# Optimization experiments

Hardware: AMD Instinct MI355X
Metric: run time of the kernel (lower is better)

## Reference

```python
import jax, jax.numpy as jnp
import numpy as np

N, E, B = 50000, 800000, 64
D_IN, D_E = 192, 64
NUM_OUT = 256


def setup_inputs() -> dict:
    key = jax.random.key(0)
    ks = jax.random.split(key, 30)
    rn = lambda k, s: jax.random.normal(k, s, dtype=jnp.float32) * 0.05
    return {
        "x": jax.random.normal(ks[0], (N, D_IN), jnp.float32),
        "edge_index": jax.random.randint(ks[1], (2, E), 0, N, dtype=jnp.int32),
        "edge_attr": jax.random.normal(ks[2], (E, D_E), jnp.float32),
        "batch": jnp.sort(jax.random.randint(ks[3], (N,), 0, B, dtype=jnp.int32)),
        "W1": rn(ks[4], (D_IN, 256)), "as1": rn(ks[5], (4, 64)), "ad1": rn(ks[6], (4, 64)),
        "We1": rn(ks[7], (D_E, 256)), "ae1": rn(ks[8], (4, 64)), "b1": rn(ks[9], (256,)),
        "W2": rn(ks[10], (256, 256)), "as2": rn(ks[11], (4, 64)), "ad2": rn(ks[12], (4, 64)),
        "We2": rn(ks[13], (D_E, 256)), "ae2": rn(ks[14], (4, 64)), "b2": rn(ks[15], (256,)),
        "W3": rn(ks[16], (256, 512)), "as3": rn(ks[17], (4, 128)), "ad3": rn(ks[18], (4, 128)),
        "We3": rn(ks[19], (D_E, 512)), "ae3": rn(ks[20], (4, 128)), "b3": rn(ks[21], (128,)),
        "Wa": rn(ks[22], (128, NUM_OUT)), "ba": rn(ks[23], (NUM_OUT,)),
        "Wv": rn(ks[24], (128, 1)), "bv": rn(ks[25], (1,)),
    }


def reference(x, edge_index, edge_attr, batch,
              W1, as1, ad1, We1, ae1, b1,
              W2, as2, ad2, We2, ae2, b2,
              W3, as3, ad3, We3, ae3, b3,
              Wa, ba, Wv, bv):
    Nn = x.shape[0]
    src0, dst0 = edge_index[0], edge_index[1]
    # PyG add_self_loops(fill_value='mean'): self-loop edge_attr = mean of incoming edge_attr
    deg = jax.ops.segment_sum(jnp.ones_like(dst0, dtype=x.dtype), dst0, num_segments=Nn)
    loop_attr = jax.ops.segment_sum(edge_attr, dst0, num_segments=Nn) / jnp.maximum(deg, 1.0)[:, None]
    loop = jnp.arange(Nn, dtype=src0.dtype)
    src = jnp.concatenate([src0, loop])
    dst = jnp.concatenate([dst0, loop])
    ea = jnp.concatenate([edge_attr, loop_attr], axis=0)

    def gat(h, W, a_s, a_d, We, a_e, bias, concat):
        Hh, C = a_s.shape
        hs = (h @ W).reshape(Nn, Hh, C)                       # [N,H,C]
        al_s = (hs * a_s).sum(-1)                             # [N,H]
        al_d = (hs * a_d).sum(-1)                             # [N,H]
        al_e = ((ea @ We).reshape(-1, Hh, C) * a_e).sum(-1)   # [E+N,H]
        alpha = jax.nn.leaky_relu(al_s[src] + al_d[dst] + al_e, 0.2)
        amax = jax.ops.segment_max(alpha, dst, num_segments=Nn)
        w = jnp.exp(alpha - amax[dst])
        denom = jax.ops.segment_sum(w, dst, num_segments=Nn)
        w = w / (denom[dst] + 1e-16)                          # scatter-softmax over dst
        out = jax.ops.segment_sum(hs[src] * w[..., None], dst, num_segments=Nn)
        out = out.reshape(Nn, Hh * C) if concat else out.mean(axis=1)
        return out + bias

    h = jax.nn.relu(gat(x, W1, as1, ad1, We1, ae1, b1, True))
    h = jax.nn.relu(gat(h, W2, as2, ad2, We2, ae2, b2, True))
    h = gat(h, W3, as3, ad3, We3, ae3, b3, False)
    cnt = jax.ops.segment_sum(jnp.ones((Nn,), h.dtype), batch, num_segments=B)
    g = jax.ops.segment_sum(h, batch, num_segments=B) / jnp.maximum(cnt, 1.0)[:, None]
    logits = g @ Wa + ba
    value = g @ Wv + bv
    return jnp.concatenate([logits, value], axis=-1)  # [B, num_outputs+1]
```

## Files before the change

kernel.cpp:

```cpp
#include <hip/hip_runtime.h>
#include <hip/hip_bf16.h>


typedef __attribute__((ext_vector_type(8))) short short8;
typedef __attribute__((ext_vector_type(4))) float floatx4;

#define DEV __device__ __forceinline__

DEV unsigned short f2b(float f) {
  union { float f; unsigned u; } v; v.f = f;
  unsigned r = v.u + 0x7FFFu + ((v.u >> 16) & 1u);
  return (unsigned short)(r >> 16);
}
DEV float b2f(unsigned short u) {
  union { unsigned u; float f; } v; v.u = ((unsigned)u) << 16;
  return v.f;
}

__global__ void k_deg(const int* __restrict__ dst, int* __restrict__ deg, int E) {
  int e = blockIdx.x * 256 + threadIdx.x;
  if (e < E) atomicAdd(&deg[dst[e]], 1);
}

__global__ __launch_bounds__(256) void k_scan1(const int* __restrict__ deg,
    int* __restrict__ rowptr, int* __restrict__ bsum, int N) {
  __shared__ int sd[256];
  int b = blockIdx.x, tid = threadIdx.x;
  int i0 = b * 1024 + tid * 4;
  int v[4]; int s = 0;
#pragma unroll
  for (int j = 0; j < 4; j++) { int i = i0 + j; v[j] = (i < N) ? deg[i] : 0; s += v[j]; }
  sd[tid] = s;
  __syncthreads();
  for (int off = 1; off < 256; off <<= 1) {
    int t = (tid >= off) ? sd[tid - off] : 0;
    __syncthreads();
    sd[tid] += t;
    __syncthreads();
  }
  int run = sd[tid] - s;
#pragma unroll
  for (int j = 0; j < 4; j++) { int i = i0 + j; if (i < N) rowptr[i] = run; run += v[j]; }
  if (tid == 255) bsum[b] = sd[255];
}

__global__ __launch_bounds__(256) void k_scan2(int* __restrict__ bsum, int nb) {
  __shared__ int sd[256];
  int tid = threadIdx.x;
  int v = (tid < nb) ? bsum[tid] : 0;
  sd[tid] = v;
  __syncthreads();
  for (int off = 1; off < 256; off <<= 1) {
    int t = (tid >= off) ? sd[tid - off] : 0;
    __syncthreads();
    sd[tid] += t;
    __syncthreads();
  }
  if (tid < nb) bsum[tid] = sd[tid] - v;
}

__global__ __launch_bounds__(256) void k_scan3(int* __restrict__ rowptr,
    int* __restrict__ cursor, const int* __restrict__ bsum, int N, int E) {
  int b = blockIdx.x, tid = threadIdx.x;
  int add = bsum[b];
  int i0 = b * 1024 + tid * 4;
#pragma unroll
  for (int j = 0; j < 4; j++) {
    int i = i0 + j;
    if (i < N) { int r = rowptr[i] + add; rowptr[i] = r; cursor[i] = r; }
  }
  if (b == 0 && tid == 0) rowptr[N] = E;
}

__global__ void k_scatter(const int* __restrict__ src, const int* __restrict__ dst,
    int* __restrict__ cursor, int2* __restrict__ csr, int E) {
  int e = blockIdx.x * 256 + threadIdx.x;
  if (e < E) {
    int d = dst[e];
    int pos = atomicAdd(&cursor[d], 1);
    csr[pos] = make_int2(src[e], e);
  }
}

__global__ void k_wt(const float* __restrict__ W, unsigned short* __restrict__ Wt,
                     int K, int Nout) {
  int idx = blockIdx.x * 256 + threadIdx.x;
  if (idx < K * Nout) {
    int n = idx / K, k = idx - n * K;
    Wt[idx] = f2b(W[(size_t)k * Nout + n]);
  }
}

__global__ void k_wep(const float* __restrict__ We1, const float* __restrict__ ae1,
                      const float* __restrict__ We2, const float* __restrict__ ae2,
                      const float* __restrict__ We3, const float* __restrict__ ae3,
                      unsigned short* __restrict__ Wept) {
  int t = blockIdx.x * 256 + threadIdx.x;
  int j = t >> 6, c = t & 63;
  int L = j >> 2, h = j & 3;
  const float* We = (L == 0) ? We1 : (L == 1) ? We2 : We3;
  const float* ae = (L == 0) ? ae1 : (L == 1) ? ae2 : ae3;
  int C = (L == 2) ? 128 : 64;
  int HC = 4 * C;
  float s = 0.f;
  for (int cc = 0; cc < C; cc++) s += We[(size_t)c * HC + h * C + cc] * ae[h * C + cc];
  Wept[j * 64 + c] = f2b(s);
  if (t < 256) {
    int jj = 12 + (t >> 6);
    Wept[jj * 64 + (t & 63)] = 0;
  }
}

template<bool A_F32, int OUT_MODE, bool DO_ALD>
__global__ __launch_bounds__(256) void k_gemm(const void* __restrict__ Ap,
    const unsigned short* __restrict__ Bt, void* __restrict__ Cp,
    int M, int Nout, int K,
    const float* __restrict__ a_s, const float* __restrict__ a_d,
    float* __restrict__ als, float* __restrict__ ald) {
  __shared__ unsigned short As[64][40];
  __shared__ unsigned short Bs[64][40];
  const int tid = threadIdx.x;
  const int wave = tid >> 6, lane = tid & 63;
  const int quad = lane >> 4, l16 = lane & 15;
  const int m0 = blockIdx.x * 64, n0 = blockIdx.y * 64;
  const int arow = tid >> 2, acg = (tid & 3) * 8;
  floatx4 acc[4] = {{0,0,0,0},{0,0,0,0},{0,0,0,0},{0,0,0,0}};
  for (int k0 = 0; k0 < K; k0 += 32) {
    {
      int gm = m0 + arow;
      unsigned short tmp[8];
      if (A_F32) {
        const float* Af = (const float*)Ap;
        if (gm < M) {
          const float4* p = (const float4*)(Af + (size_t)gm * K + k0 + acg);
          float4 u0 = p[0], u1 = p[1];
          tmp[0]=f2b(u0.x); tmp[1]=f2b(u0.y); tmp[2]=f2b(u0.z); tmp[3]=f2b(u0.w);
          tmp[4]=f2b(u1.x); tmp[5]=f2b(u1.y); tmp[6]=f2b(u1.z); tmp[7]=f2b(u1.w);
        } else {
#pragma unroll
          for (int j = 0; j < 8; j++) tmp[j] = 0;
        }
      } else {
        const unsigned short* Ab = (const unsigned short*)Ap;
        uint4 u = {0,0,0,0};
        if (gm < M) u = *(const uint4*)(Ab + (size_t)gm * K + k0 + acg);
        *(uint4*)tmp = u;
      }
      *(uint4*)&As[arow][acg] = *(uint4*)tmp;
      int gn = n0 + arow;
      uint4 bv = {0,0,0,0};
      if (gn < Nout) bv = *(const uint4*)(Bt + (size_t)gn * K + k0 + acg);
      *(uint4*)&Bs[arow][acg] = bv;
    }
    __syncthreads();
    short8 a = *(const short8*)&As[wave * 16 + l16][quad * 8];
#pragma unroll
    for (int t = 0; t < 4; t++) {
      short8 b = *(const short8*)&Bs[t * 16 + l16][quad * 8];
      acc[t] = __builtin_amdgcn_mfma_f32_16x16x32_bf16(a, b, acc[t], 0, 0, 0);
    }
    __syncthreads();
  }
#pragma unroll
  for (int t = 0; t < 4; t++) {
#pragma unroll
    for (int r = 0; r < 4; r++) {
      int row = m0 + wave * 16 + quad * 4 + r;
      int col = n0 + t * 16 + l16;
      float v = acc[t][r];
      if (OUT_MODE == 0) {
        if (row < M && col < Nout)
          ((unsigned short*)Cp)[(size_t)row * Nout + col] = f2b(v);
      } else {
        if (row < M && col < 12)
          ((float*)Cp)[(size_t)row * 16 + col] = v;
      }
    }
  }
  if constexpr (DO_ALD) {
    int h = (n0 * 4) / Nout;
#pragma unroll
    for (int r = 0; r < 4; r++) {
      float ps = 0.f, pd = 0.f;
#pragma unroll
      for (int t = 0; t < 4; t++) {
        int col = n0 + t * 16 + l16;
        float v = acc[t][r];
        ps += v * a_s[col];
        pd += v * a_d[col];
      }
#pragma unroll
      for (int off = 1; off < 16; off <<= 1) {
        ps += __shfl_xor(ps, off, 64);
        pd += __shfl_xor(pd, off, 64);
      }
      int row = m0 + wave * 16 + quad * 4 + r;
      if (l16 == 0 && row < M) {
        atomicAdd(&als[row * 4 + h], ps);
        atomicAdd(&ald[row * 4 + h], pd);
      }
    }
  }
}

__global__ __launch_bounds__(256) void k_loop_ale(const int* __restrict__ rowptr,
    const int2* __restrict__ csr, float* __restrict__ ale, int N, int E) {
  int t = blockIdx.x * 256 + threadIdx.x;
  int node = t >> 2, q = t & 3;
  if (node >= N) return;
  int s = rowptr[node], e = rowptr[node + 1];
  float4 a = make_float4(0.f, 0.f, 0.f, 0.f);
  if (q < 3) {
    for (int p = s; p < e; p++) {
      int eid = csr[p].y;
      float4 v = *(const float4*)(ale + (size_t)eid * 16 + q * 4);
      a.x += v.x; a.y += v.y; a.z += v.z; a.w += v.w;
    }
  }
  float inv = 1.0f / (float)((e - s) > 1 ? (e - s) : 1);
  if (q < 3)
    *(float4*)(ale + ((size_t)E + node) * 16 + q * 4) =
        make_float4(a.x * inv, a.y * inv, a.z * inv, a.w * inv);
}

template<int LPN, int VPL, int MODE>
__global__ __launch_bounds__(256) void k_gath(const unsigned short* __restrict__ hs,
    const int* __restrict__ rowptr, const int2* __restrict__ csr,
    const float* __restrict__ ale,
    int L4,
    const float* __restrict__ als, const float* __restrict__ ald,
    const float* __restrict__ bias, unsigned short* __restrict__ outb,
    float* __restrict__ outf, int N, int E) {
  constexpr int U = 4;
  constexpr int NV = VPL / 8;
  constexpr int HC = LPN * VPL;
  constexpr int SH = (LPN == 8) ? 1 : 2;
  constexpr int NPB = 256 / LPN;
  const int lane = threadIdx.x & 63;
  const int sl = lane & (LPN - 1);
  const int grp = lane / LPN;
  const int hd = sl >> SH;
  const int node = blockIdx.x * NPB + (threadIdx.x >> 6) * (64 / LPN) + grp;
  if (node >= N) return;
  const int start = rowptr[node];
  const int cnt = rowptr[node + 1] - start;
  const float aldh = ald[node * 4 + hd];
  float acc[VPL];
#pragma unroll
  for (int j = 0; j < VPL; j++) acc[j] = 0.f;
  float den = 0.f;
  for (int base = 0; base < cnt; base += U) {
    int sp[U]; float pw[U];
#pragma unroll
    for (int e = 0; e < U; e++) {
      int idx = base + e;
      int idc = idx < cnt ? idx : cnt - 1;
      int2 se = csr[start + idc];
      sp[e] = se.x;
      float av = als[(size_t)se.x * 4 + hd] + aldh +
                 ale[(size_t)se.y * 16 + L4 + hd];
      av = av > 0.f ? av : 0.2f * av;
      float p = __expf(av);
      pw[e] = idx < cnt ? p : 0.f;
    }
    uint4 dv[U][NV];
#pragma unroll
    for (int e = 0; e < U; e++) {
      const uint4* rp = (const uint4*)(hs + (size_t)sp[e] * HC + sl * VPL);
#pragma unroll
      for (int q = 0; q < NV; q++) dv[e][q] = rp[q];
    }
#pragma unroll
    for (int e = 0; e < U; e++) {
      den += pw[e];
      const unsigned short* vs = (const unsigned short*)&dv[e][0];
#pragma unroll
      for (int j = 0; j < VPL; j++) acc[j] += pw[e] * b2f(vs[j]);
    }
  }
  {
    float av = als[(size_t)node * 4 + hd] + aldh +
               ale[((size_t)E + node) * 16 + L4 + hd];
    av = av > 0.f ? av : 0.2f * av;
    float p = __expf(av);
    den += p;
    const uint4* rp = (const uint4*)(hs + (size_t)node * HC + sl * VPL);
#pragma unroll
    for (int q = 0; q < NV; q++) {
      uint4 u = rp[q];
      const unsigned short* vs = (const unsigned short*)&u;
#pragma unroll
      for (int j = 0; j < 8; j++) acc[q * 8 + j] += p * b2f(vs[j]);
    }
  }
  float inv = 1.0f / (den + 1e-16f);
  if constexpr (MODE == 0) {
    unsigned short tmp[VPL];
#pragma unroll
    for (int j = 0; j < VPL; j++) {
      float v = acc[j] * inv + bias[sl * VPL + j];
      tmp[j] = f2b(fmaxf(v, 0.f));
    }
    unsigned short* op = outb + (size_t)node * HC + sl * VPL;
#pragma unroll
    for (int q = 0; q < NV; q++) ((uint4*)op)[q] = ((uint4*)tmp)[q];
  } else {
#pragma unroll
    for (int j = 0; j < VPL; j++) {
      float v = acc[j] * inv;
      v += __shfl_xor(v, 4, 64);
      v += __shfl_xor(v, 8, 64);
      acc[j] = v * 0.25f;
    }
    if (sl < 4) {
      float* op = outf + (size_t)node * (4 * VPL) + sl * VPL;
#pragma unroll
      for (int j = 0; j < VPL; j++) op[j] = acc[j] + bias[sl * VPL + j];
    }
  }
}

__global__ __launch_bounds__(256) void k_pool(const float* __restrict__ out3,
    const int* __restrict__ bat, float* __restrict__ g, int* __restrict__ cntb, int N) {
  int wid = blockIdx.x * 4 + (threadIdx.x >> 6);
  int lane = threadIdx.x & 63;
  int per = (N + 255) / 256;
  int s = wid * per, e = s + per;
  if (e > N) e = N;
  if (s >= e) return;
  int cur = bat[s];
  float ax = 0.f, ay = 0.f; int run = 0;
  for (int n = s; n < e; n++) {
    int b = bat[n];
    if (b != cur) {
      atomicAdd(&g[cur * 128 + lane * 2], ax);
      atomicAdd(&g[cur * 128 + lane * 2 + 1], ay);
      if (lane == 0) atomicAdd(&cntb[cur], run);
      ax = 0.f; ay = 0.f; run = 0; cur = b;
    }
    float2 v = *(const float2*)(out3 + (size_t)n * 128 + lane * 2);
    ax += v.x; ay += v.y; run++;
  }
  atomicAdd(&g[cur * 128 + lane * 2], ax);
  atomicAdd(&g[cur * 128 + lane * 2 + 1], ay);
  if (lane == 0) atomicAdd(&cntb[cur], run);
}

__global__ __launch_bounds__(320) void k_final(const float* __restrict__ g,
    const int* __restrict__ cntb, const float* __restrict__ Wa, const float* __restrict__ ba,
    const float* __restrict__ Wv, const float* __restrict__ bv, float* __restrict__ out) {
  __shared__ float gm[128];
  int b = blockIdx.x, t = threadIdx.x;
  if (t < 128) {
    float c = (float)cntb[b];
    gm[t] = g[b * 128 + t] / fmaxf(c, 1.f);
  }
  __syncthreads();
  if (t < 257) {
    float acc = 0.f;
    if (t < 256) {
      for (int k = 0; k < 128; k++) acc += gm[k] * Wa[k * 256 + t];
      acc += ba[t];
    } else {
      for (int k = 0; k < 128; k++) acc += gm[k] * Wv[k];
      acc += bv[0];
    }
    out[b * 257 + t] = acc;
  }
}

extern "C" void kernel_launch(void* const* d_in, const int* in_sizes, int n_in,
                              void* d_out, int out_size, void* d_ws, size_t ws_size,
                              hipStream_t stream) {
  const float* x   = (const float*)d_in[0];
  const int*   ei  = (const int*)  d_in[1];
  const float* ea  = (const float*)d_in[2];
  const int*   bat = (const int*)  d_in[3];
  const float* W1  = (const float*)d_in[4];
  const float* as1 = (const float*)d_in[5];
  const float* ad1 = (const float*)d_in[6];
  const float* We1 = (const float*)d_in[7];
  const float* ae1 = (const float*)d_in[8];
  const float* b1  = (const float*)d_in[9];
  const float* W2  = (const float*)d_in[10];
  const float* as2 = (const float*)d_in[11];
  const float* ad2 = (const float*)d_in[12];
  const float* We2 = (const float*)d_in[13];
  const float* ae2 = (const float*)d_in[14];
  const float* b2  = (const float*)d_in[15];
  const float* W3  = (const float*)d_in[16];
  const float* as3 = (const float*)d_in[17];
  const float* ad3 = (const float*)d_in[18];
  const float* We3 = (const float*)d_in[19];
  const float* ae3 = (const float*)d_in[20];
  const float* b3  = (const float*)d_in[21];
  const float* Wa  = (const float*)d_in[22];
  const float* ba  = (const float*)d_in[23];
  const float* Wv  = (const float*)d_in[24];
  const float* bv  = (const float*)d_in[25];
  (void)n_in; (void)out_size; (void)ws_size;

  const int N = in_sizes[0] / 192;
  const int E = in_sizes[1] / 2;
  const size_t EN = (size_t)E + N;
  const int* srcv = ei;
  const int* dstv = ei + E;
  const int nb = (N + 1023) / 1024;

  size_t off = 0;
  auto alloc = [&](size_t bytes) -> char* {
    char* p = (char*)d_ws + off;
    off += (bytes + 255) & ~(size_t)255;
    return p;
  };
  int* deg     = (int*)alloc((size_t)N * 4);
  int* rowptr  = (int*)alloc((size_t)(N + 1) * 4);
  int* cursor  = (int*)alloc((size_t)N * 4);
  int* bsum    = (int*)alloc(256 * 4);
  int2* csr    = (int2*)alloc((size_t)E * 8);
  float* ale   = (float*)alloc(EN * 16 * 4);
  unsigned short* Wept = (unsigned short*)alloc(16 * 64 * 2);
  unsigned short* W1t  = (unsigned short*)alloc(256 * 192 * 2);
  unsigned short* W2t  = (unsigned short*)alloc(256 * 256 * 2);
  unsigned short* W3t  = (unsigned short*)alloc(512 * 256 * 2);
  unsigned short* hs   = (unsigned short*)alloc((size_t)N * 512 * 2);
  unsigned short* h1   = (unsigned short*)alloc((size_t)N * 256 * 2);
  unsigned short* h2   = (unsigned short*)alloc((size_t)N * 256 * 2);
  float* out3  = (float*)alloc((size_t)N * 128 * 4);
  float* als_all = (float*)alloc((size_t)N * 4 * 4 * 6);
  float* g     = (float*)alloc(64 * 128 * 4 + 64 * 4);
  int* cntb    = (int*)(g + 64 * 128);
  float* als1 = als_all + (size_t)N * 4 * 0;
  float* ald1 = als_all + (size_t)N * 4 * 1;
  float* als2 = als_all + (size_t)N * 4 * 2;
  float* ald2 = als_all + (size_t)N * 4 * 3;
  float* als3 = als_all + (size_t)N * 4 * 4;
  float* ald3 = als_all + (size_t)N * 4 * 5;

  hipMemsetAsync(deg, 0, (size_t)N * 4, stream);
  hipMemsetAsync(als_all, 0, (size_t)N * 4 * 4 * 6, stream);
  hipMemsetAsync(g, 0, 64 * 128 * 4 + 64 * 4, stream);

  k_deg<<<(E + 255) / 256, 256, 0, stream>>>(dstv, deg, E);
  k_scan1<<<nb, 256, 0, stream>>>(deg, rowptr, bsum, N);
  k_scan2<<<1, 256, 0, stream>>>(bsum, nb);
  k_scan3<<<nb, 256, 0, stream>>>(rowptr, cursor, bsum, N, E);
  k_scatter<<<(E + 255) / 256, 256, 0, stream>>>(srcv, dstv, cursor, csr, E);
  k_wt<<<(192 * 256 + 255) / 256, 256, 0, stream>>>(W1, W1t, 192, 256);
  k_wt<<<(256 * 256 + 255) / 256, 256, 0, stream>>>(W2, W2t, 256, 256);
  k_wt<<<(256 * 512 + 255) / 256, 256, 0, stream>>>(W3, W3t, 256, 512);
  k_wep<<<3, 256, 0, stream>>>(We1, ae1, We2, ae2, We3, ae3, Wept);
  k_gemm<true, 2, false><<<dim3((E + 63) / 64, 1), 256, 0, stream>>>(
      ea, Wept, ale, E, 16, 64, nullptr, nullptr, nullptr, nullptr);
  k_loop_ale<<<(N * 4 + 255) / 256, 256, 0, stream>>>(rowptr, csr, ale, N, E);
  k_gemm<true, 0, true><<<dim3((N + 63) / 64, 4), 256, 0, stream>>>(
      x, W1t, hs, N, 256, 192, as1, ad1, als1, ald1);
  k_gath<8, 32, 0><<<(N + 31) / 32, 256, 0, stream>>>(
      hs, rowptr, csr, ale, 0, als1, ald1, b1, h1, nullptr, N, E);
  k_gemm<false, 0, true><<<dim3((N + 63) / 64, 4), 256, 0, stream>>>(
      h1, W2t, hs, N, 256, 256, as2, ad2, als2, ald2);
  k_gath<8, 32, 0><<<(N + 31) / 32, 256, 0, stream>>>(
      hs, rowptr, csr, ale, 4, als2, ald2, b2, h2, nullptr, N, E);
  k_gemm<false, 0, true><<<dim3((N + 63) / 64, 8), 256, 0, stream>>>(
      h2, W3t, hs, N, 512, 256, as3, ad3, als3, ald3);
  k_gath<16, 32, 1><<<(N + 15) / 16, 256, 0, stream>>>(
      hs, rowptr, csr, ale, 8, als3, ald3, b3, nullptr, out3, N, E);
  k_pool<<<64, 256, 0, stream>>>(out3, bat, g, cntb, N);
  k_final<<<64, 320, 0, stream>>>(g, cntb, Wa, ba, Wv, bv, (float*)d_out);
}
```

Baseline: 1.067 ms.

## Store per-layer edge attention in CSR order and balance gather nodes dynamically

The edge-attention GEMM now scatters its per-layer results straight into CSR-ordered arrays, one per layer, through a position array recorded during the CSR scatter. The gather kernels and the self-loop mean then read edge logits contiguously, with no indirection through the edge id, and the CSR holds only source ids. The gather kernels also take nodes from a shared-memory atomic counter, 64 nodes per block, so lane groups with short neighbour lists pick up more work. This adds a scattered write in the edge GEMM and an extra E-sized index array.

```diff
diff --git a/kernel.cpp b/kernel.cpp
--- a/kernel.cpp
+++ b/kernel.cpp
@@ -73,12 +73,13 @@
 }
 
 __global__ void k_scatter(const int* __restrict__ src, const int* __restrict__ dst,
-    int* __restrict__ cursor, int2* __restrict__ csr, int E) {
+    int* __restrict__ cursor, int* __restrict__ csr_src, int* __restrict__ posArr, int E) {
   int e = blockIdx.x * 256 + threadIdx.x;
   if (e < E) {
     int d = dst[e];
     int pos = atomicAdd(&cursor[d], 1);
-    csr[pos] = make_int2(src[e], e);
+    csr_src[pos] = src[e];
+    posArr[e] = pos;
   }
 }
 
@@ -116,7 +117,9 @@
     const unsigned short* __restrict__ Bt, void* __restrict__ Cp,
     int M, int Nout, int K,
     const float* __restrict__ a_s, const float* __restrict__ a_d,
-    float* __restrict__ als, float* __restrict__ ald) {
+    float* __restrict__ als, float* __restrict__ ald,
+    const int* __restrict__ posArr,
+    float* __restrict__ aleP0, float* __restrict__ aleP1, float* __restrict__ aleP2) {
   __shared__ unsigned short As[64][40];
   __shared__ unsigned short Bs[64][40];
   const int tid = threadIdx.x;
@@ -161,19 +164,26 @@
     }
     __syncthreads();
   }
-#pragma unroll
-  for (int t = 0; t < 4; t++) {
+  if (OUT_MODE == 0) {
+#pragma unroll
+    for (int t = 0; t < 4; t++) {
+#pragma unroll
+      for (int r = 0; r < 4; r++) {
+        int row = m0 + wave * 16 + quad * 4 + r;
+        int col = n0 + t * 16 + l16;
+        if (row < M && col < Nout)
+          ((unsigned short*)Cp)[(size_t)row * Nout + col] = f2b(acc[t][r]);
+      }
+    }
+  } else {
 #pragma unroll
     for (int r = 0; r < 4; r++) {
       int row = m0 + wave * 16 + quad * 4 + r;
-      int col = n0 + t * 16 + l16;
-      float v = acc[t][r];
-      if (OUT_MODE == 0) {
-        if (row < M && col < Nout)
-          ((unsigned short*)Cp)[(size_t)row * Nout + col] = f2b(v);
-      } else {
-        if (row < M && col < 12)
-          ((float*)Cp)[(size_t)row * 16 + col] = v;
+      int col = l16;
+      if (row < M && col < 12) {
+        int pos = posArr[row];
+        float* dstp = (col < 4) ? aleP0 : (col < 8) ? aleP1 : aleP2;
+        dstp[(size_t)pos * 4 + (col & 3)] = acc[0][r];
       }
     }
   }
@@ -204,118 +214,125 @@
 }
 
 __global__ __launch_bounds__(256) void k_loop_ale(const int* __restrict__ rowptr,
-    const int2* __restrict__ csr, float* __restrict__ ale, int N, int E) {
+    float* __restrict__ aleP0, float* __restrict__ aleP1, float* __restrict__ aleP2,
+    int N, int E) {
   int t = blockIdx.x * 256 + threadIdx.x;
   int node = t >> 2, q = t & 3;
-  if (node >= N) return;
+  if (node >= N || q >= 3) return;
+  float* aleP = (q == 0) ? aleP0 : (q == 1) ? aleP1 : aleP2;
   int s = rowptr[node], e = rowptr[node + 1];
   float4 a = make_float4(0.f, 0.f, 0.f, 0.f);
-  if (q < 3) {
-    for (int p = s; p < e; p++) {
-      int eid = csr[p].y;
-      float4 v = *(const float4*)(ale + (size_t)eid * 16 + q * 4);
-      a.x += v.x; a.y += v.y; a.z += v.z; a.w += v.w;
-    }
+  for (int p = s; p < e; p++) {
+    float4 v = *(const float4*)(aleP + (size_t)p * 4);
+    a.x += v.x; a.y += v.y; a.z += v.z; a.w += v.w;
   }
   float inv = 1.0f / (float)((e - s) > 1 ? (e - s) : 1);
-  if (q < 3)
-    *(float4*)(ale + ((size_t)E + node) * 16 + q * 4) =
-        make_float4(a.x * inv, a.y * inv, a.z * inv, a.w * inv);
-}
-
-template<int LPN, int VPL, int MODE>
+  *(float4*)(aleP + ((size_t)E + node) * 4) =
+      make_float4(a.x * inv, a.y * inv, a.z * inv, a.w * inv);
+}
+
+template<int LPN, int MODE>
 __global__ __launch_bounds__(256) void k_gath(const unsigned short* __restrict__ hs,
-    const int* __restrict__ rowptr, const int2* __restrict__ csr,
-    const float* __restrict__ ale,
-    int L4,
+    const int* __restrict__ rowptr, const int* __restrict__ csr_src,
+    const float* __restrict__ aleP,
     const float* __restrict__ als, const float* __restrict__ ald,
     const float* __restrict__ bias, unsigned short* __restrict__ outb,
     float* __restrict__ outf, int N, int E) {
   constexpr int U = 4;
-  constexpr int NV = VPL / 8;
+  constexpr int VPL = 32;
+  constexpr int NV = 4;
   constexpr int HC = LPN * VPL;
   constexpr int SH = (LPN == 8) ? 1 : 2;
-  constexpr int NPB = 256 / LPN;
-  const int lane = threadIdx.x & 63;
+  constexpr int NPB = 64;
+  __shared__ int s_ctr;
+  const int tid = threadIdx.x;
+  if (tid == 0) s_ctr = 0;
+  __syncthreads();
+  const int lane = tid & 63;
   const int sl = lane & (LPN - 1);
-  const int grp = lane / LPN;
+  const int base_lane = lane & ~(LPN - 1);
   const int hd = sl >> SH;
-  const int node = blockIdx.x * NPB + (threadIdx.x >> 6) * (64 / LPN) + grp;
-  if (node >= N) return;
-  const int start = rowptr[node];
-  const int cnt = rowptr[node + 1] - start;
-  const float aldh = ald[node * 4 + hd];
-  float acc[VPL];
-#pragma unroll
-  for (int j = 0; j < VPL; j++) acc[j] = 0.f;
-  float den = 0.f;
-  for (int base = 0; base < cnt; base += U) {
-    int sp[U]; float pw[U];
-#pragma unroll
-    for (int e = 0; e < U; e++) {
-      int idx = base + e;
-      int idc = idx < cnt ? idx : cnt - 1;
-      int2 se = csr[start + idc];
-      sp[e] = se.x;
-      float av = als[(size_t)se.x * 4 + hd] + aldh +
-                 ale[(size_t)se.y * 16 + L4 + hd];
+  for (;;) {
+    int it = 0;
+    if (sl == 0) it = atomicAdd(&s_ctr, 1);
+    it = __shfl(it, base_lane, 64);
+    if (it >= NPB) break;
+    const int node = blockIdx.x * NPB + it;
+    if (node >= N) break;
+    const int start = rowptr[node];
+    const int cnt = rowptr[node + 1] - start;
+    const float aldh = ald[node * 4 + hd];
+    float acc[VPL];
+#pragma unroll
+    for (int j = 0; j < VPL; j++) acc[j] = 0.f;
+    float den = 0.f;
+    for (int base = 0; base < cnt; base += U) {
+      int sp[U]; float pw[U];
+#pragma unroll
+      for (int e = 0; e < U; e++) {
+        int idx = base + e;
+        int idc = idx < cnt ? idx : cnt - 1;
+        sp[e] = csr_src[start + idc];
+        float av = als[(size_t)sp[e] * 4 + hd] + aldh +
+                   aleP[(size_t)(start + idc) * 4 + hd];
+        av = av > 0.f ? av : 0.2f * av;
+        float p = __expf(av);
+        pw[e] = idx < cnt ? p : 0.f;
+      }
+      uint4 dv[U][NV];
+#pragma unroll
+      for (int e = 0; e < U; e++) {
+        const uint4* rp = (const uint4*)(hs + (size_t)sp[e] * HC + sl * VPL);
+#pragma unroll
+        for (int q = 0; q < NV; q++) dv[e][q] = rp[q];
+      }
+#pragma unroll
+      for (int e = 0; e < U; e++) {
+        den += pw[e];
+        const unsigned short* vs = (const unsigned short*)&dv[e][0];
+#pragma unroll
+        for (int j = 0; j < VPL; j++) acc[j] += pw[e] * b2f(vs[j]);
+      }
+    }
+    {
+      float av = als[(size_t)node * 4 + hd] + aldh +
+                 aleP[((size_t)E + node) * 4 + hd];
       av = av > 0.f ? av : 0.2f * av;
       float p = __expf(av);
-      pw[e] = idx < cnt ? p : 0.f;
-    }
-    uint4 dv[U][NV];
-#pragma unroll
-    for (int e = 0; e < U; e++) {
-      const uint4* rp = (const uint4*)(hs + (size_t)sp[e] * HC + sl * VPL);
-#pragma unroll
-      for (int q = 0; q < NV; q++) dv[e][q] = rp[q];
-    }
-#pragma unroll
-    for (int e = 0; e < U; e++) {
-      den += pw[e];
-      const unsigned short* vs = (const unsigned short*)&dv[e][0];
-#pragma unroll
-      for (int j = 0; j < VPL; j++) acc[j] += pw[e] * b2f(vs[j]);
-    }
-  }
-  {
-    float av = als[(size_t)node * 4 + hd] + aldh +
-               ale[((size_t)E + node) * 16 + L4 + hd];
-    av = av > 0.f ? av : 0.2f * av;
-    float p = __expf(av);
-    den += p;
-    const uint4* rp = (const uint4*)(hs + (size_t)node * HC + sl * VPL);
-#pragma unroll
-    for (int q = 0; q < NV; q++) {
-      uint4 u = rp[q];
-      const unsigned short* vs = (const unsigned short*)&u;
-#pragma unroll
-      for (int j = 0; j < 8; j++) acc[q * 8 + j] += p * b2f(vs[j]);
-    }
-  }
-  float inv = 1.0f / (den + 1e-16f);
-  if constexpr (MODE == 0) {
-    unsigned short tmp[VPL];
-#pragma unroll
-    for (int j = 0; j < VPL; j++) {
-      float v = acc[j] * inv + bias[sl * VPL + j];
-      tmp[j] = f2b(fmaxf(v, 0.f));
-    }
-    unsigned short* op = outb + (size_t)node * HC + sl * VPL;
-#pragma unroll
-    for (int q = 0; q < NV; q++) ((uint4*)op)[q] = ((uint4*)tmp)[q];
-  } else {
-#pragma unroll
-    for (int j = 0; j < VPL; j++) {
-      float v = acc[j] * inv;
-      v += __shfl_xor(v, 4, 64);
-      v += __shfl_xor(v, 8, 64);
-      acc[j] = v * 0.25f;
-    }
-    if (sl < 4) {
-      float* op = outf + (size_t)node * (4 * VPL) + sl * VPL;
-#pragma unroll
-      for (int j = 0; j < VPL; j++) op[j] = acc[j] + bias[sl * VPL + j];
+      den += p;
+      const uint4* rp = (const uint4*)(hs + (size_t)node * HC + sl * VPL);
+#pragma unroll
+      for (int q = 0; q < NV; q++) {
+        uint4 u = rp[q];
+        const unsigned short* vs = (const unsigned short*)&u;
+#pragma unroll
+        for (int j = 0; j < 8; j++) acc[q * 8 + j] += p * b2f(vs[j]);
+      }
+    }
+    float inv = 1.0f / (den + 1e-16f);
+    if constexpr (MODE == 0) {
+      unsigned short tmp[VPL];
+#pragma unroll
+      for (int j = 0; j < VPL; j++) {
+        float v = acc[j] * inv + bias[sl * VPL + j];
+        tmp[j] = f2b(fmaxf(v, 0.f));
+      }
+      unsigned short* op = outb + (size_t)node * HC + sl * VPL;
+#pragma unroll
+      for (int q = 0; q < NV; q++) ((uint4*)op)[q] = ((uint4*)tmp)[q];
+    } else {
+#pragma unroll
+      for (int j = 0; j < VPL; j++) {
+        float v = acc[j] * inv;
+        v += __shfl_xor(v, 4, 64);
+        v += __shfl_xor(v, 8, 64);
+        acc[j] = v * 0.25f;
+      }
+      if (sl < 4) {
+        float* op = outf + (size_t)node * (4 * VPL) + sl * VPL;
+#pragma unroll
+        for (int j = 0; j < VPL; j++) op[j] = acc[j] + bias[sl * VPL + j];
+      }
     }
   }
 }
@@ -402,7 +419,6 @@
 
   const int N = in_sizes[0] / 192;
   const int E = in_sizes[1] / 2;
-  const size_t EN = (size_t)E + N;
   const int* srcv = ei;
   const int* dstv = ei + E;
   const int nb = (N + 1023) / 1024;
@@ -417,8 +433,11 @@
   int* rowptr  = (int*)alloc((size_t)(N + 1) * 4);
   int* cursor  = (int*)alloc((size_t)N * 4);
   int* bsum    = (int*)alloc(256 * 4);
-  int2* csr    = (int2*)alloc((size_t)E * 8);
-  float* ale   = (float*)alloc(EN * 16 * 4);
+  int* csr_src = (int*)alloc((size_t)E * 4);
+  int* posArr  = (int*)alloc((size_t)E * 4);
+  float* aleP0 = (float*)alloc((size_t)(E + N) * 16);
+  float* aleP1 = (float*)alloc((size_t)(E + N) * 16);
+  float* aleP2 = (float*)alloc((size_t)(E + N) * 16);
   unsigned short* Wept = (unsigned short*)alloc(16 * 64 * 2);
   unsigned short* W1t  = (unsigned short*)alloc(256 * 192 * 2);
   unsigned short* W2t  = (unsigned short*)alloc(256 * 256 * 2);
@@ -445,26 +464,27 @@
   k_scan1<<<nb, 256, 0, stream>>>(deg, rowptr, bsum, N);
   k_scan2<<<1, 256, 0, stream>>>(bsum, nb);
   k_scan3<<<nb, 256, 0, stream>>>(rowptr, cursor, bsum, N, E);
-  k_scatter<<<(E + 255) / 256, 256, 0, stream>>>(srcv, dstv, cursor, csr, E);
+  k_scatter<<<(E + 255) / 256, 256, 0, stream>>>(srcv, dstv, cursor, csr_src, posArr, E);
   k_wt<<<(192 * 256 + 255) / 256, 256, 0, stream>>>(W1, W1t, 192, 256);
   k_wt<<<(256 * 256 + 255) / 256, 256, 0, stream>>>(W2, W2t, 256, 256);
   k_wt<<<(256 * 512 + 255) / 256, 256, 0, stream>>>(W3, W3t, 256, 512);
   k_wep<<<3, 256, 0, stream>>>(We1, ae1, We2, ae2, We3, ae3, Wept);
   k_gemm<true, 2, false><<<dim3((E + 63) / 64, 1), 256, 0, stream>>>(
-      ea, Wept, ale, E, 16, 64, nullptr, nullptr, nullptr, nullptr);
-  k_loop_ale<<<(N * 4 + 255) / 256, 256, 0, stream>>>(rowptr, csr, ale, N, E);
+      ea, Wept, nullptr, E, 16, 64, nullptr, nullptr, nullptr, nullptr,
+      posArr, aleP0, aleP1, aleP2);
+  k_loop_ale<<<(N * 4 + 255) / 256, 256, 0, stream>>>(rowptr, aleP0, aleP1, aleP2, N, E);
   k_gemm<true, 0, true><<<dim3((N + 63) / 64, 4), 256, 0, stream>>>(
-      x, W1t, hs, N, 256, 192, as1, ad1, als1, ald1);
-  k_gath<8, 32, 0><<<(N + 31) / 32, 256, 0, stream>>>(
-      hs, rowptr, csr, ale, 0, als1, ald1, b1, h1, nullptr, N, E);
+      x, W1t, hs, N, 256, 192, as1, ad1, als1, ald1, nullptr, nullptr, nullptr, nullptr);
+  k_gath<8, 0><<<(N + 63) / 64, 256, 0, stream>>>(
+      hs, rowptr, csr_src, aleP0, als1, ald1, b1, h1, nullptr, N, E);
   k_gemm<false, 0, true><<<dim3((N + 63) / 64, 4), 256, 0, stream>>>(
-      h1, W2t, hs, N, 256, 256, as2, ad2, als2, ald2);
-  k_gath<8, 32, 0><<<(N + 31) / 32, 256, 0, stream>>>(
-      hs, rowptr, csr, ale, 4, als2, ald2, b2, h2, nullptr, N, E);
+      h1, W2t, hs, N, 256, 256, as2, ad2, als2, ald2, nullptr, nullptr, nullptr, nullptr);
+  k_gath<8, 0><<<(N + 63) / 64, 256, 0, stream>>>(
+      hs, rowptr, csr_src, aleP1, als2, ald2, b2, h2, nullptr, N, E);
   k_gemm<false, 0, true><<<dim3((N + 63) / 64, 8), 256, 0, stream>>>(
-      h2, W3t, hs, N, 512, 256, as3, ad3, als3, ald3);
-  k_gath<16, 32, 1><<<(N + 15) / 16, 256, 0, stream>>>(
-      hs, rowptr, csr, ale, 8, als3, ald3, b3, nullptr, out3, N, E);
+      h2, W3t, hs, N, 512, 256, as3, ad3, als3, ald3, nullptr, nullptr, nullptr, nullptr);
+  k_gath<16, 1><<<(N + 63) / 64, 256, 0, stream>>>(
+      hs, rowptr, csr_src, aleP2, als3, ald3, b3, nullptr, out3, N, E);
   k_pool<<<64, 256, 0, stream>>>(out3, bat, g, cntb, N);
   k_final<<<64, 320, 0, stream>>>(g, cntb, Wa, ba, Wv, bv, (float*)d_out);
 }
```

Result: slower. 1.090 ms (+2.2%).
